# Performance work log

Hardware: AMD Instinct MI355X
Metric: run time of the kernel (lower is better)

The kernel has to match this reference:

```python
import jax, jax.numpy as jnp
import numpy as np

H = 12        # heads
D = 768       # d_model
DK = D // H   # per-head dim
B, S = 1, 4096


def setup_inputs() -> dict:
    key = jax.random.key(0)
    ks = jax.random.split(key, 8)
    scale = 1.0 / np.sqrt(D)
    return {
        "q": jax.random.normal(ks[0], (B, S, D), jnp.float32),
        "k": jax.random.normal(ks[1], (B, S, D), jnp.float32),
        "v": jax.random.normal(ks[2], (B, S, D), jnp.float32),
        "Wq": jax.random.normal(ks[3], (D, D), jnp.float32) * scale,
        "bq": jnp.zeros((D,), jnp.float32),
        "Wk": jax.random.normal(ks[4], (D, D), jnp.float32) * scale,
        "bk": jnp.zeros((D,), jnp.float32),
        "Wv": jax.random.normal(ks[5], (D, D), jnp.float32) * scale,
        "bv": jnp.zeros((D,), jnp.float32),
        "Wo": jax.random.normal(ks[6], (D, D), jnp.float32) * scale,
        "bo": jnp.zeros((D,), jnp.float32),
    }


def reference(q, k, v, Wq, bq, Wk, bk, Wv, bv, Wo, bo):
    bs, sq, _ = q.shape
    sk = k.shape[1]
    # projections, then split heads: (b, h, s, dk)
    qh = (q @ Wq + bq).reshape(bs, sq, H, DK).transpose(0, 2, 1, 3)
    kh = (k @ Wk + bk).reshape(bs, sk, H, DK).transpose(0, 2, 1, 3)
    vh = (v @ Wv + bv).reshape(bs, sk, H, DK).transpose(0, 2, 1, 3)
    # scaled dot-product attention (mask=None, dropout inactive)
    scores = jnp.einsum("bhqd,bhkd->bhqk", qh, kh) / jnp.sqrt(jnp.float32(DK))
    attn = jax.nn.softmax(scores, axis=-1)
    ctx = jnp.einsum("bhqk,bhkd->bhqd", attn, vh)
    concat = ctx.transpose(0, 2, 1, 3).reshape(bs, sq, D)
    return concat @ Wo + bo
```

## Files before the change

kernel.cpp:

```cpp
#include <hip/hip_runtime.h>
#include <hip/hip_bf16.h>


constexpr int S_LEN = 4096;
constexpr int D_MODEL = 768;
constexpr int N_HEADS = 12;
constexpr int D_HEAD = 64;
constexpr int SEG = 2;
constexpr int SEG_LEN = S_LEN / SEG;
constexpr int NITER = SEG_LEN / 64;

#define QSCALE 0.180336880111120f

typedef _Float16 f16;
typedef __attribute__((ext_vector_type(8))) _Float16 f16x8;
typedef __attribute__((ext_vector_type(4))) _Float16 f16x4;
typedef __attribute__((ext_vector_type(4))) float f32x4;

__global__ __launch_bounds__(256) void prep_kernel(
    const float* __restrict__ q, const float* __restrict__ k,
    const float* __restrict__ v, f16* __restrict__ qh,
    f16* __restrict__ kh, f16* __restrict__ vh,
    const float* __restrict__ W0, const float* __restrict__ W1,
    const float* __restrict__ W2, const float* __restrict__ W3,
    f16* __restrict__ WtBase)
{
    __shared__ float T[64][65];
    int bid = blockIdx.x;
    const int t = threadIdx.x;
    if (bid < 4608) {
        int g = bid / 1536, r = bid % 1536;
        const float* x = (g == 0) ? q : (g == 1) ? k : v;
        f16* y = (g == 0) ? qh : (g == 1) ? kh : vh;
        int i = (r * 256 + t) * 8;
        float4 a = *(const float4*)&x[i];
        float4 b = *(const float4*)&x[i + 4];
        f16x8 h = { (f16)a.x, (f16)a.y, (f16)a.z, (f16)a.w,
                    (f16)b.x, (f16)b.y, (f16)b.z, (f16)b.w };
        *(f16x8*)&y[i] = h;
        return;
    }
    bid -= 4608;
    int g = bid / 144, r = bid % 144;
    const float* W = (g == 0) ? W0 : (g == 1) ? W1 : (g == 2) ? W2 : W3;
    f16* Wt = WtBase + (size_t)g * D_MODEL * D_MODEL;
    const int r0 = (r / 12) * 64;
    const int c0 = (r % 12) * 64;
    #pragma unroll
    for (int i = 0; i < 16; ++i) {
        int e = t + 256 * i; int rr = e >> 6, cc = e & 63;
        T[rr][cc] = W[(size_t)(r0 + rr) * D_MODEL + c0 + cc];
    }
    __syncthreads();
    #pragma unroll
    for (int i = 0; i < 16; ++i) {
        int e = t + 256 * i; int rr = e >> 6, cc = e & 63;
        Wt[(size_t)(c0 + rr) * D_MODEL + r0 + cc] = (f16)T[cc][rr];
    }
}

#define GSTR 72

__device__ __forceinline__ void gemm128_core(
    const f16* __restrict__ A, const f16* __restrict__ B,
    f16* As, f16* Bs, int K, int row0, int col0, int t, f32x4 acc[4][4])
{
    const int w = t >> 6, l = t & 63, quad = l >> 4, l15 = l & 15;
    const int wm = (w & 1) * 64, wn = (w >> 1) * 64;

    f16x8 pa[4], pb[4];
    #pragma unroll
    for (int i = 0; i < 4; ++i) {
        int idx = i * 256 + t;
        int r = idx >> 3, c = (idx & 7) * 8;
        pa[i] = *(const f16x8*)&A[(size_t)(row0 + r) * K + c];
        pb[i] = *(const f16x8*)&B[(size_t)(col0 + r) * K + c];
    }

    for (int k0 = 0; k0 < K; k0 += 64) {
        __syncthreads();
        #pragma unroll
        for (int i = 0; i < 4; ++i) {
            int idx = i * 256 + t;
            int r = idx >> 3, c = (idx & 7) * 8;
            *(f16x8*)&As[r * GSTR + c] = pa[i];
            *(f16x8*)&Bs[r * GSTR + c] = pb[i];
        }
        __syncthreads();

        int kn = k0 + 64;
        if (kn < K) {
            #pragma unroll
            for (int i = 0; i < 4; ++i) {
                int idx = i * 256 + t;
                int r = idx >> 3, c = (idx & 7) * 8;
                pa[i] = *(const f16x8*)&A[(size_t)(row0 + r) * K + kn + c];
                pb[i] = *(const f16x8*)&B[(size_t)(col0 + r) * K + kn + c];
            }
        }

        #pragma unroll
        for (int kc = 0; kc < 2; ++kc) {
            f16x8 af[4], bf[4];
            #pragma unroll
            for (int mt = 0; mt < 4; ++mt)
                af[mt] = *(f16x8*)&As[(wm + mt * 16 + l15) * GSTR + kc * 32 + quad * 8];
            #pragma unroll
            for (int nt = 0; nt < 4; ++nt)
                bf[nt] = *(f16x8*)&Bs[(wn + nt * 16 + l15) * GSTR + kc * 32 + quad * 8];
            #pragma unroll
            for (int mt = 0; mt < 4; ++mt)
                #pragma unroll
                for (int nt = 0; nt < 4; ++nt)
                    acc[mt][nt] = __builtin_amdgcn_mfma_f32_16x16x32_f16(
                        af[mt], bf[nt], acc[mt][nt], 0, 0, 0);
        }
    }
}

__global__ __launch_bounds__(256) void qkv_gemm_kernel(
    const f16* __restrict__ qh, const f16* __restrict__ kh,
    const f16* __restrict__ vh, const f16* __restrict__ WtBase,
    const float* __restrict__ bq, const float* __restrict__ bk,
    const float* __restrict__ bv,
    f16* __restrict__ Qp, f16* __restrict__ Kp, f16* __restrict__ Vpt)
{
    __shared__ f16 As[128 * GSTR];
    __shared__ f16 Bs[128 * GSTR];
    const size_t DD = (size_t)D_MODEL * D_MODEL;
    int bid = blockIdx.x;
    int g = bid / 192, r = bid % 192;

    const f16 *A, *B; const float* bias; f16* Y;
    int N; bool biasRow; float scale;
    int row0, col0;
    if (g == 0) {
        A = qh; B = WtBase; bias = bq; Y = Qp;
        N = D_MODEL; biasRow = false; scale = QSCALE;
        row0 = (r / 6) * 128; col0 = (r % 6) * 128;
    } else if (g == 1) {
        A = kh; B = WtBase + DD; bias = bk; Y = Kp;
        N = D_MODEL; biasRow = false; scale = 1.0f;
        row0 = (r / 6) * 128; col0 = (r % 6) * 128;
    } else {
        A = WtBase + 2 * DD; B = vh; bias = bv; Y = Vpt;
        N = S_LEN; biasRow = true; scale = 1.0f;
        row0 = (r / 32) * 128; col0 = (r % 32) * 128;
    }

    f32x4 acc[4][4];
    #pragma unroll
    for (int i = 0; i < 4; ++i)
        #pragma unroll
        for (int j = 0; j < 4; ++j) acc[i][j] = (f32x4){0.f, 0.f, 0.f, 0.f};

    const int t = threadIdx.x;
    gemm128_core(A, B, As, Bs, D_MODEL, row0, col0, t, acc);

    const int w = t >> 6, l = t & 63, quad = l >> 4, l15 = l & 15;
    const int wm = (w & 1) * 64, wn = (w >> 1) * 64;
    #pragma unroll
    for (int mt = 0; mt < 4; ++mt) {
        #pragma unroll
        for (int nt = 0; nt < 4; ++nt) {
            int col = col0 + wn + nt * 16 + l15;
            #pragma unroll
            for (int reg = 0; reg < 4; ++reg) {
                int row = row0 + wm + mt * 16 + quad * 4 + reg;
                float b = biasRow ? bias[row] : bias[col];
                Y[(size_t)row * N + col] = (f16)((acc[mt][nt][reg] + b) * scale);
            }
        }
    }
}

#define LSTR 72

__global__ __launch_bounds__(256, 4) void flash_attn_part_kernel(
    const f16* __restrict__ Q, const f16* __restrict__ K,
    const f16* __restrict__ Vg, f16* __restrict__ Opart,
    float* __restrict__ lsum)
{
    __shared__ f16 Ks[2][64 * LSTR];
    __shared__ f16 Vt[2][64 * LSTR];

    const int t    = threadIdx.x;
    const int w    = t >> 6;
    const int l    = t & 63;
    const int quad = l >> 4;
    const int l15  = l & 15;
    const int h    = blockIdx.y;
    const int q0   = blockIdx.x * 128;
    const int seg  = blockIdx.z;
    const int c0   = h * D_HEAD;
    const size_t SD = (size_t)S_LEN * D_MODEL;

    const int sr = t >> 3;
    const int sc = (t & 7) * 8;
    const int srk = ((sr & 4) << 2) | ((sr & 24) >> 1) | (sr & 3);

    f16x8 qa[2][2];
    #pragma unroll
    for (int qt = 0; qt < 2; ++qt) {
        const f16* qrow = Q + (size_t)(q0 + w * 32 + qt * 16 + l15) * D_MODEL + c0;
        qa[qt][0] = *(const f16x8*)&qrow[quad * 8];
        qa[qt][1] = *(const f16x8*)&qrow[32 + quad * 8];
    }

    f32x4 ctx[2][4];
    float lAcc[2] = {0.f, 0.f};
    #pragma unroll
    for (int qt = 0; qt < 2; ++qt)
        #pragma unroll
        for (int i = 0; i < 4; ++i) ctx[qt][i] = (f32x4){0.f, 0.f, 0.f, 0.f};

    const int kt0 = seg * SEG_LEN;

    f16x8 kreg[2], vreg[2];
    #pragma unroll
    for (int i = 0; i < 2; ++i) {
        int r = i * 32 + sr;
        kreg[i] = *(const f16x8*)&K[(size_t)(kt0 + r) * D_MODEL + c0 + sc];
        vreg[i] = *(const f16x8*)&Vg[(size_t)(c0 + r) * S_LEN + kt0 + sc];
    }
    #pragma unroll
    for (int i = 0; i < 2; ++i) {
        int r = i * 32 + sr;
        *(f16x8*)&Ks[0][(i * 32 + srk) * LSTR + sc] = kreg[i];
        *(f16x8*)&Vt[0][r * LSTR + sc] = vreg[i];
    }
    __syncthreads();
    #pragma unroll
    for (int i = 0; i < 2; ++i) {
        int r = i * 32 + sr;
        kreg[i] = *(const f16x8*)&K[(size_t)(kt0 + 64 + r) * D_MODEL + c0 + sc];
        vreg[i] = *(const f16x8*)&Vg[(size_t)(c0 + r) * S_LEN + kt0 + 64 + sc];
    }

    for (int it = 0; it < NITER; ++it) {
        const int buf = it & 1;
        const f16* ks = Ks[buf];
        const f16* vt = Vt[buf];

        f16x8 pf[2][2];
        #pragma unroll
        for (int s = 0; s < 4; ++s) {
            const int kslot = s >> 1, half = s & 1;
            const f16* kr = &ks[(kslot * 32 + half * 16 + l15) * LSTR];
            f16x8 kb0 = *(const f16x8*)&kr[quad * 8];
            f16x8 kb1 = *(const f16x8*)&kr[32 + quad * 8];
            #pragma unroll
            for (int qt = 0; qt < 2; ++qt) {
                f32x4 z = (f32x4){0.f, 0.f, 0.f, 0.f};
                z = __builtin_amdgcn_mfma_f32_16x16x32_f16(kb0, qa[qt][0], z, 0, 0, 0);
                z = __builtin_amdgcn_mfma_f32_16x16x32_f16(kb1, qa[qt][1], z, 0, 0, 0);
                float p0 = __builtin_amdgcn_exp2f(z[0]);
                float p1 = __builtin_amdgcn_exp2f(z[1]);
                float p2 = __builtin_amdgcn_exp2f(z[2]);
                float p3 = __builtin_amdgcn_exp2f(z[3]);
                lAcc[qt] += (p0 + p1) + (p2 + p3);
                pf[qt][kslot][half * 4 + 0] = (f16)p0;
                pf[qt][kslot][half * 4 + 1] = (f16)p1;
                pf[qt][kslot][half * 4 + 2] = (f16)p2;
                pf[qt][kslot][half * 4 + 3] = (f16)p3;
            }
        }

        #pragma unroll
        for (int mt = 0; mt < 4; ++mt) {
            #pragma unroll
            for (int ks2 = 0; ks2 < 2; ++ks2) {
                f16x8 va = *(const f16x8*)&vt[(mt * 16 + l15) * LSTR + ks2 * 32 + quad * 8];
                #pragma unroll
                for (int qt = 0; qt < 2; ++qt)
                    ctx[qt][mt] = __builtin_amdgcn_mfma_f32_16x16x32_f16(
                        va, pf[qt][ks2], ctx[qt][mt], 0, 0, 0);
            }
        }

        if (it + 1 < NITER) {
            #pragma unroll
            for (int i = 0; i < 2; ++i) {
                int r = i * 32 + sr;
                *(f16x8*)&Ks[1 - buf][(i * 32 + srk) * LSTR + sc] = kreg[i];
                *(f16x8*)&Vt[1 - buf][r * LSTR + sc] = vreg[i];
            }
        }
        __syncthreads();

        if (it + 2 < NITER) {
            int ktn = kt0 + (it + 2) * 64;
            #pragma unroll
            for (int i = 0; i < 2; ++i) {
                int r = i * 32 + sr;
                kreg[i] = *(const f16x8*)&K[(size_t)(ktn + r) * D_MODEL + c0 + sc];
                vreg[i] = *(const f16x8*)&Vg[(size_t)(c0 + r) * S_LEN + ktn + sc];
            }
        }
    }

    #pragma unroll
    for (int qt = 0; qt < 2; ++qt) {
        int qrow = q0 + w * 32 + qt * 16 + l15;
        #pragma unroll
        for (int mt = 0; mt < 4; ++mt) {
            f16x4 ov = { (f16)ctx[qt][mt][0], (f16)ctx[qt][mt][1],
                         (f16)ctx[qt][mt][2], (f16)ctx[qt][mt][3] };
            *(f16x4*)&Opart[(size_t)seg * SD + (size_t)qrow * D_MODEL
                            + c0 + mt * 16 + quad * 4] = ov;
        }
        float s = lAcc[qt];
        s += __shfl_xor(s, 16);
        s += __shfl_xor(s, 32);
        if (quad == 0)
            lsum[((size_t)seg * N_HEADS + h) * S_LEN + qrow] = s;
    }
}

__global__ __launch_bounds__(256) void combine_kernel(
    const f16* __restrict__ Opart, const float* __restrict__ lsum,
    f16* __restrict__ Ctx)
{
    const size_t SD = (size_t)S_LEN * D_MODEL;
    int tid = blockIdx.x * 256 + threadIdx.x;
    int idx = tid * 8;
    int row = idx / D_MODEL;
    int c   = idx % D_MODEL;
    int h   = c >> 6;
    float l0 = lsum[(size_t)h * S_LEN + row];
    float l1 = lsum[((size_t)N_HEADS + h) * S_LEN + row];
    float inv = 1.0f / (l0 + l1);
    f16x8 o0 = *(const f16x8*)&Opart[(size_t)row * D_MODEL + c];
    f16x8 o1 = *(const f16x8*)&Opart[SD + (size_t)row * D_MODEL + c];
    f16x8 r;
    #pragma unroll
    for (int j = 0; j < 8; ++j)
        r[j] = (f16)(((float)o0[j] + (float)o1[j]) * inv);
    *(f16x8*)&Ctx[(size_t)row * D_MODEL + c] = r;
}

__global__ __launch_bounds__(256) void oproj_kernel(
    const f16* __restrict__ Ctx, const f16* __restrict__ Wto,
    const float* __restrict__ bo, float* __restrict__ out)
{
    __shared__ f16 As[128 * GSTR];
    __shared__ f16 Bs[128 * GSTR];
    int bid = blockIdx.x;
    int row0 = (bid / 6) * 128, col0 = (bid % 6) * 128;

    f32x4 acc[4][4];
    #pragma unroll
    for (int i = 0; i < 4; ++i)
        #pragma unroll
        for (int j = 0; j < 4; ++j) acc[i][j] = (f32x4){0.f, 0.f, 0.f, 0.f};

    const int t = threadIdx.x;
    gemm128_core(Ctx, Wto, As, Bs, D_MODEL, row0, col0, t, acc);

    const int w = t >> 6, l = t & 63, quad = l >> 4, l15 = l & 15;
    const int wm = (w & 1) * 64, wn = (w >> 1) * 64;
    #pragma unroll
    for (int mt = 0; mt < 4; ++mt) {
        #pragma unroll
        for (int nt = 0; nt < 4; ++nt) {
            int col = col0 + wn + nt * 16 + l15;
            float b = bo[col];
            #pragma unroll
            for (int reg = 0; reg < 4; ++reg) {
                int row = row0 + wm + mt * 16 + quad * 4 + reg;
                out[(size_t)row * D_MODEL + col] = acc[mt][nt][reg] + b;
            }
        }
    }
}

extern "C" void kernel_launch(void* const* d_in, const int* in_sizes, int n_in,
                              void* d_out, int out_size, void* d_ws, size_t ws_size,
                              hipStream_t stream)
{
    const float* q  = (const float*)d_in[0];
    const float* k  = (const float*)d_in[1];
    const float* v  = (const float*)d_in[2];
    const float* Wq = (const float*)d_in[3];
    const float* bq = (const float*)d_in[4];
    const float* Wk = (const float*)d_in[5];
    const float* bk = (const float*)d_in[6];
    const float* Wv = (const float*)d_in[7];
    const float* bv = (const float*)d_in[8];
    const float* Wo = (const float*)d_in[9];
    const float* bo = (const float*)d_in[10];
    float* out = (float*)d_out;

    const size_t SD = (size_t)S_LEN * D_MODEL;
    const size_t DD = (size_t)D_MODEL * D_MODEL;
    f16* base   = (f16*)d_ws;
    f16* WtBase = base;
    f16* Wto    = WtBase + 3 * DD;
    f16* Qp     = base + 4 * DD;
    f16* Kp     = Qp + SD;
    f16* Vpt    = Kp + SD;
    f16* qh     = Vpt + SD;
    f16* kh     = qh + SD;
    f16* vh     = kh + SD;
    f16* Opart  = qh;
    f16* Ctx    = qh + 2 * SD;
    float* lsum = (float*)(base + 4 * DD + 6 * SD);

    prep_kernel<<<3 * 1536 + 4 * 144, 256, 0, stream>>>(
        q, k, v, qh, kh, vh, Wq, Wk, Wv, Wo, WtBase);

    qkv_gemm_kernel<<<3 * 192, 256, 0, stream>>>(
        qh, kh, vh, WtBase, bq, bk, bv, Qp, Kp, Vpt);

    dim3 gAttn(S_LEN / 128, N_HEADS, SEG);
    flash_attn_part_kernel<<<gAttn, 256, 0, stream>>>(Qp, Kp, Vpt, Opart, lsum);

    combine_kernel<<<1536, 256, 0, stream>>>(Opart, lsum, Ctx);

    oproj_kernel<<<192, 256, 0, stream>>>(Ctx, Wto, bo, out);
}
```

Before: 210.0 us.

## Split attention into four key segments with 32-key tiles and higher occupancy

Attention now uses 32-key tiles instead of 64, which halves the shared-memory K/V buffers, and the occupancy hint rises from 4 to 6 blocks per CU. The number of key segments becomes a runtime value, set to 4 when the workspace is large enough, so the grid has more blocks to fill the GPU. The combine kernel sums a variable number of partials and writes the result in place into segment 0's buffer. The cost is a larger partial buffer and combine traffic, plus twice as many barriers per key, each covering less MFMA work.

```diff
diff --git a/kernel.cpp b/kernel.cpp
--- a/kernel.cpp
+++ b/kernel.cpp
@@ -6,9 +6,6 @@
 constexpr int D_MODEL = 768;
 constexpr int N_HEADS = 12;
 constexpr int D_HEAD = 64;
-constexpr int SEG = 2;
-constexpr int SEG_LEN = S_LEN / SEG;
-constexpr int NITER = SEG_LEN / 64;
 
 #define QSCALE 0.180336880111120f
 
@@ -174,15 +171,16 @@
     }
 }
 
-#define LSTR 72
-
-__global__ __launch_bounds__(256, 4) void flash_attn_part_kernel(
+#define LSTRK 72
+#define VSTR  36
+
+__global__ __launch_bounds__(256, 6) void flash_attn_part_kernel(
     const f16* __restrict__ Q, const f16* __restrict__ K,
     const f16* __restrict__ Vg, f16* __restrict__ Opart,
-    float* __restrict__ lsum)
-{
-    __shared__ f16 Ks[2][64 * LSTR];
-    __shared__ f16 Vt[2][64 * LSTR];
+    float* __restrict__ lsum, int seg_len)
+{
+    __shared__ f16 Ks[2][32 * LSTRK];
+    __shared__ f16 Vt[2][64 * VSTR];
 
     const int t    = threadIdx.x;
     const int w    = t >> 6;
@@ -194,10 +192,13 @@
     const int seg  = blockIdx.z;
     const int c0   = h * D_HEAD;
     const size_t SD = (size_t)S_LEN * D_MODEL;
-
-    const int sr = t >> 3;
-    const int sc = (t & 7) * 8;
+    const int NIT  = seg_len >> 5;
+
+    const int sr  = t >> 3;
+    const int sc  = (t & 7) * 8;
     const int srk = ((sr & 4) << 2) | ((sr & 24) >> 1) | (sr & 3);
+    const int svr = t >> 2;
+    const int svc = (t & 3) * 8;
 
     f16x8 qa[2][2];
     #pragma unroll
@@ -214,39 +215,26 @@
         #pragma unroll
         for (int i = 0; i < 4; ++i) ctx[qt][i] = (f32x4){0.f, 0.f, 0.f, 0.f};
 
-    const int kt0 = seg * SEG_LEN;
-
-    f16x8 kreg[2], vreg[2];
-    #pragma unroll
-    for (int i = 0; i < 2; ++i) {
-        int r = i * 32 + sr;
-        kreg[i] = *(const f16x8*)&K[(size_t)(kt0 + r) * D_MODEL + c0 + sc];
-        vreg[i] = *(const f16x8*)&Vg[(size_t)(c0 + r) * S_LEN + kt0 + sc];
-    }
-    #pragma unroll
-    for (int i = 0; i < 2; ++i) {
-        int r = i * 32 + sr;
-        *(f16x8*)&Ks[0][(i * 32 + srk) * LSTR + sc] = kreg[i];
-        *(f16x8*)&Vt[0][r * LSTR + sc] = vreg[i];
-    }
+    const int kt0 = seg * seg_len;
+
+    f16x8 kreg, vreg;
+    kreg = *(const f16x8*)&K[(size_t)(kt0 + sr) * D_MODEL + c0 + sc];
+    vreg = *(const f16x8*)&Vg[(size_t)(c0 + svr) * S_LEN + kt0 + svc];
+    *(f16x8*)&Ks[0][srk * LSTRK + sc] = kreg;
+    *(f16x8*)&Vt[0][svr * VSTR + svc] = vreg;
     __syncthreads();
-    #pragma unroll
-    for (int i = 0; i < 2; ++i) {
-        int r = i * 32 + sr;
-        kreg[i] = *(const f16x8*)&K[(size_t)(kt0 + 64 + r) * D_MODEL + c0 + sc];
-        vreg[i] = *(const f16x8*)&Vg[(size_t)(c0 + r) * S_LEN + kt0 + 64 + sc];
-    }
-
-    for (int it = 0; it < NITER; ++it) {
+    kreg = *(const f16x8*)&K[(size_t)(kt0 + 32 + sr) * D_MODEL + c0 + sc];
+    vreg = *(const f16x8*)&Vg[(size_t)(c0 + svr) * S_LEN + kt0 + 32 + svc];
+
+    for (int it = 0; it < NIT; ++it) {
         const int buf = it & 1;
         const f16* ks = Ks[buf];
         const f16* vt = Vt[buf];
 
-        f16x8 pf[2][2];
-        #pragma unroll
-        for (int s = 0; s < 4; ++s) {
-            const int kslot = s >> 1, half = s & 1;
-            const f16* kr = &ks[(kslot * 32 + half * 16 + l15) * LSTR];
+        f16x8 pf[2];
+        #pragma unroll
+        for (int half = 0; half < 2; ++half) {
+            const f16* kr = &ks[(half * 16 + l15) * LSTRK];
             f16x8 kb0 = *(const f16x8*)&kr[quad * 8];
             f16x8 kb1 = *(const f16x8*)&kr[32 + quad * 8];
             #pragma unroll
@@ -259,43 +247,32 @@
                 float p2 = __builtin_amdgcn_exp2f(z[2]);
                 float p3 = __builtin_amdgcn_exp2f(z[3]);
                 lAcc[qt] += (p0 + p1) + (p2 + p3);
-                pf[qt][kslot][half * 4 + 0] = (f16)p0;
-                pf[qt][kslot][half * 4 + 1] = (f16)p1;
-                pf[qt][kslot][half * 4 + 2] = (f16)p2;
-                pf[qt][kslot][half * 4 + 3] = (f16)p3;
+                pf[qt][half * 4 + 0] = (f16)p0;
+                pf[qt][half * 4 + 1] = (f16)p1;
+                pf[qt][half * 4 + 2] = (f16)p2;
+                pf[qt][half * 4 + 3] = (f16)p3;
             }
         }
 
         #pragma unroll
         for (int mt = 0; mt < 4; ++mt) {
-            #pragma unroll
-            for (int ks2 = 0; ks2 < 2; ++ks2) {
-                f16x8 va = *(const f16x8*)&vt[(mt * 16 + l15) * LSTR + ks2 * 32 + quad * 8];
-                #pragma unroll
-                for (int qt = 0; qt < 2; ++qt)
-                    ctx[qt][mt] = __builtin_amdgcn_mfma_f32_16x16x32_f16(
-                        va, pf[qt][ks2], ctx[qt][mt], 0, 0, 0);
-            }
-        }
-
-        if (it + 1 < NITER) {
-            #pragma unroll
-            for (int i = 0; i < 2; ++i) {
-                int r = i * 32 + sr;
-                *(f16x8*)&Ks[1 - buf][(i * 32 + srk) * LSTR + sc] = kreg[i];
-                *(f16x8*)&Vt[1 - buf][r * LSTR + sc] = vreg[i];
-            }
+            f16x8 va = *(const f16x8*)&vt[(mt * 16 + l15) * VSTR + quad * 8];
+            #pragma unroll
+            for (int qt = 0; qt < 2; ++qt)
+                ctx[qt][mt] = __builtin_amdgcn_mfma_f32_16x16x32_f16(
+                    va, pf[qt], ctx[qt][mt], 0, 0, 0);
+        }
+
+        if (it + 1 < NIT) {
+            *(f16x8*)&Ks[1 - buf][srk * LSTRK + sc] = kreg;
+            *(f16x8*)&Vt[1 - buf][svr * VSTR + svc] = vreg;
         }
         __syncthreads();
 
-        if (it + 2 < NITER) {
-            int ktn = kt0 + (it + 2) * 64;
-            #pragma unroll
-            for (int i = 0; i < 2; ++i) {
-                int r = i * 32 + sr;
-                kreg[i] = *(const f16x8*)&K[(size_t)(ktn + r) * D_MODEL + c0 + sc];
-                vreg[i] = *(const f16x8*)&Vg[(size_t)(c0 + r) * S_LEN + ktn + sc];
-            }
+        if (it + 2 < NIT) {
+            int ktn = kt0 + (it + 2) * 32;
+            kreg = *(const f16x8*)&K[(size_t)(ktn + sr) * D_MODEL + c0 + sc];
+            vreg = *(const f16x8*)&Vg[(size_t)(c0 + svr) * S_LEN + ktn + svc];
         }
     }
 
@@ -318,25 +295,29 @@
 }
 
 __global__ __launch_bounds__(256) void combine_kernel(
-    const f16* __restrict__ Opart, const float* __restrict__ lsum,
-    f16* __restrict__ Ctx)
+    f16* Opart, const float* __restrict__ lsum, int nseg)
 {
     const size_t SD = (size_t)S_LEN * D_MODEL;
     int tid = blockIdx.x * 256 + threadIdx.x;
     int idx = tid * 8;
     int row = idx / D_MODEL;
     int c   = idx % D_MODEL;
-    int h   = c >> 6;
-    float l0 = lsum[(size_t)h * S_LEN + row];
-    float l1 = lsum[((size_t)N_HEADS + h) * S_LEN + row];
-    float inv = 1.0f / (l0 + l1);
-    f16x8 o0 = *(const f16x8*)&Opart[(size_t)row * D_MODEL + c];
-    f16x8 o1 = *(const f16x8*)&Opart[SD + (size_t)row * D_MODEL + c];
+    int hh  = c >> 6;
+    float lt = 0.f;
+    for (int s = 0; s < nseg; ++s)
+        lt += lsum[((size_t)s * N_HEADS + hh) * S_LEN + row];
+    float inv = 1.0f / lt;
+    float o[8] = {0.f, 0.f, 0.f, 0.f, 0.f, 0.f, 0.f, 0.f};
+    for (int s = 0; s < nseg; ++s) {
+        f16x8 os = *(const f16x8*)&Opart[(size_t)s * SD + (size_t)row * D_MODEL + c];
+        #pragma unroll
+        for (int j = 0; j < 8; ++j) o[j] += (float)os[j];
+    }
     f16x8 r;
     #pragma unroll
     for (int j = 0; j < 8; ++j)
-        r[j] = (f16)(((float)o0[j] + (float)o1[j]) * inv);
-    *(f16x8*)&Ctx[(size_t)row * D_MODEL + c] = r;
+        r[j] = (f16)(o[j] * inv);
+    *(f16x8*)&Opart[(size_t)row * D_MODEL + c] = r;
 }
 
 __global__ __launch_bounds__(256) void oproj_kernel(
@@ -403,8 +384,12 @@
     f16* kh     = qh + SD;
     f16* vh     = kh + SD;
     f16* Opart  = qh;
-    f16* Ctx    = qh + 2 * SD;
-    float* lsum = (float*)(base + 4 * DD + 6 * SD);
+
+    const size_t need4 = (4 * DD + 7 * SD) * sizeof(f16)
+                       + 4 * (size_t)N_HEADS * S_LEN * sizeof(float);
+    const int nseg = (ws_size >= need4) ? 4 : 2;
+    const int seg_len = S_LEN / nseg;
+    float* lsum = (float*)(base + 4 * DD + (3 + (size_t)nseg) * SD);
 
     prep_kernel<<<3 * 1536 + 4 * 144, 256, 0, stream>>>(
         q, k, v, qh, kh, vh, Wq, Wk, Wv, Wo, WtBase);
@@ -412,10 +397,11 @@
     qkv_gemm_kernel<<<3 * 192, 256, 0, stream>>>(
         qh, kh, vh, WtBase, bq, bk, bv, Qp, Kp, Vpt);
 
-    dim3 gAttn(S_LEN / 128, N_HEADS, SEG);
-    flash_attn_part_kernel<<<gAttn, 256, 0, stream>>>(Qp, Kp, Vpt, Opart, lsum);
-
-    combine_kernel<<<1536, 256, 0, stream>>>(Opart, lsum, Ctx);
-
-    oproj_kernel<<<192, 256, 0, stream>>>(Ctx, Wto, bo, out);
-}
+    dim3 gAttn(S_LEN / 128, N_HEADS, nseg);
+    flash_attn_part_kernel<<<gAttn, 256, 0, stream>>>(
+        Qp, Kp, Vpt, Opart, lsum, seg_len);
+
+    combine_kernel<<<1536, 256, 0, stream>>>(Opart, lsum, nseg);
+
+    oproj_kernel<<<192, 256, 0, stream>>>(Opart, Wto, bo, out);
+}
```

Measured after the change: 335.2 us. +59.6%, slower.

## Fuse fp32→fp16 input conversion into QKV GEMM and split-combine into O-proj loads

Applied to the files above, without the earlier changes.

The separate pass that converted q/k/v from fp32 to fp16 is removed. The QKV GEMM now loads fp32 tiles directly and converts them in registers. The combine kernel is also removed: the output-projection GEMM reads both partial attention outputs plus the lsum values and normalizes them while loading its A operand. This cuts two kernel launches and several full S×D intermediate round trips through global memory. In exchange the GEMM loads fetch twice the bytes for fp32 operands, and the O-proj repeats the combine work for each of its 6 column tiles, with extra lsum loads and divides.

```diff
diff --git a/kernel.cpp b/kernel.cpp
--- a/kernel.cpp
+++ b/kernel.cpp
@@ -18,9 +18,6 @@
 typedef __attribute__((ext_vector_type(4))) float f32x4;
 
 __global__ __launch_bounds__(256) void prep_kernel(
-    const float* __restrict__ q, const float* __restrict__ k,
-    const float* __restrict__ v, f16* __restrict__ qh,
-    f16* __restrict__ kh, f16* __restrict__ vh,
     const float* __restrict__ W0, const float* __restrict__ W1,
     const float* __restrict__ W2, const float* __restrict__ W3,
     f16* __restrict__ WtBase)
@@ -28,19 +25,6 @@
     __shared__ float T[64][65];
     int bid = blockIdx.x;
     const int t = threadIdx.x;
-    if (bid < 4608) {
-        int g = bid / 1536, r = bid % 1536;
-        const float* x = (g == 0) ? q : (g == 1) ? k : v;
-        f16* y = (g == 0) ? qh : (g == 1) ? kh : vh;
-        int i = (r * 256 + t) * 8;
-        float4 a = *(const float4*)&x[i];
-        float4 b = *(const float4*)&x[i + 4];
-        f16x8 h = { (f16)a.x, (f16)a.y, (f16)a.z, (f16)a.w,
-                    (f16)b.x, (f16)b.y, (f16)b.z, (f16)b.w };
-        *(f16x8*)&y[i] = h;
-        return;
-    }
-    bid -= 4608;
     int g = bid / 144, r = bid % 144;
     const float* W = (g == 0) ? W0 : (g == 1) ? W1 : (g == 2) ? W2 : W3;
     f16* Wt = WtBase + (size_t)g * D_MODEL * D_MODEL;
@@ -61,21 +45,59 @@
 
 #define GSTR 72
 
-__device__ __forceinline__ void gemm128_core(
-    const f16* __restrict__ A, const f16* __restrict__ B,
+template<int AM, int BM>
+__device__ __forceinline__ void gemm128_core_t(
+    const f16* A16, const float* Af, const f16* A16b, const float* ls,
+    const f16* B16, const float* Bf,
     f16* As, f16* Bs, int K, int row0, int col0, int t, f32x4 acc[4][4])
 {
     const int w = t >> 6, l = t & 63, quad = l >> 4, l15 = l & 15;
     const int wm = (w & 1) * 64, wn = (w >> 1) * 64;
 
     f16x8 pa[4], pb[4];
-    #pragma unroll
-    for (int i = 0; i < 4; ++i) {
+
+    auto loadA = [&](int i, int kk) {
         int idx = i * 256 + t;
         int r = idx >> 3, c = (idx & 7) * 8;
-        pa[i] = *(const f16x8*)&A[(size_t)(row0 + r) * K + c];
-        pb[i] = *(const f16x8*)&B[(size_t)(col0 + r) * K + c];
-    }
+        if constexpr (AM == 0) {
+            pa[i] = *(const f16x8*)&A16[(size_t)(row0 + r) * K + kk + c];
+        } else if constexpr (AM == 1) {
+            const float* p = &Af[(size_t)(row0 + r) * K + kk + c];
+            float4 a = *(const float4*)p;
+            float4 b = *(const float4*)(p + 4);
+            pa[i] = (f16x8){ (f16)a.x, (f16)a.y, (f16)a.z, (f16)a.w,
+                             (f16)b.x, (f16)b.y, (f16)b.z, (f16)b.w };
+        } else {
+            int R = row0 + r;
+            f16x8 a0 = *(const f16x8*)&A16[(size_t)R * K + kk + c];
+            f16x8 a1 = *(const f16x8*)&A16b[(size_t)R * K + kk + c];
+            int hh = (kk + c) >> 6;
+            float lt = ls[(size_t)hh * S_LEN + R]
+                     + ls[(size_t)(N_HEADS + hh) * S_LEN + R];
+            float inv = 1.0f / lt;
+            f16x8 o;
+            #pragma unroll
+            for (int j = 0; j < 8; ++j)
+                o[j] = (f16)(((float)a0[j] + (float)a1[j]) * inv);
+            pa[i] = o;
+        }
+    };
+    auto loadB = [&](int i, int kk) {
+        int idx = i * 256 + t;
+        int r = idx >> 3, c = (idx & 7) * 8;
+        if constexpr (BM == 0) {
+            pb[i] = *(const f16x8*)&B16[(size_t)(col0 + r) * K + kk + c];
+        } else {
+            const float* p = &Bf[(size_t)(col0 + r) * K + kk + c];
+            float4 a = *(const float4*)p;
+            float4 b = *(const float4*)(p + 4);
+            pb[i] = (f16x8){ (f16)a.x, (f16)a.y, (f16)a.z, (f16)a.w,
+                             (f16)b.x, (f16)b.y, (f16)b.z, (f16)b.w };
+        }
+    };
+
+    #pragma unroll
+    for (int i = 0; i < 4; ++i) { loadA(i, 0); loadB(i, 0); }
 
     for (int k0 = 0; k0 < K; k0 += 64) {
         __syncthreads();
@@ -91,12 +113,7 @@
         int kn = k0 + 64;
         if (kn < K) {
             #pragma unroll
-            for (int i = 0; i < 4; ++i) {
-                int idx = i * 256 + t;
-                int r = idx >> 3, c = (idx & 7) * 8;
-                pa[i] = *(const f16x8*)&A[(size_t)(row0 + r) * K + kn + c];
-                pb[i] = *(const f16x8*)&B[(size_t)(col0 + r) * K + kn + c];
-            }
+            for (int i = 0; i < 4; ++i) { loadA(i, kn); loadB(i, kn); }
         }
 
         #pragma unroll
@@ -119,8 +136,8 @@
 }
 
 __global__ __launch_bounds__(256) void qkv_gemm_kernel(
-    const f16* __restrict__ qh, const f16* __restrict__ kh,
-    const f16* __restrict__ vh, const f16* __restrict__ WtBase,
+    const float* __restrict__ q, const float* __restrict__ k,
+    const float* __restrict__ v, const f16* __restrict__ WtBase,
     const float* __restrict__ bq, const float* __restrict__ bk,
     const float* __restrict__ bv,
     f16* __restrict__ Qp, f16* __restrict__ Kp, f16* __restrict__ Vpt)
@@ -130,32 +147,33 @@
     const size_t DD = (size_t)D_MODEL * D_MODEL;
     int bid = blockIdx.x;
     int g = bid / 192, r = bid % 192;
-
-    const f16 *A, *B; const float* bias; f16* Y;
+    const int t = threadIdx.x;
+
+    f32x4 acc[4][4];
+    #pragma unroll
+    for (int i = 0; i < 4; ++i)
+        #pragma unroll
+        for (int j = 0; j < 4; ++j) acc[i][j] = (f32x4){0.f, 0.f, 0.f, 0.f};
+
+    const float* bias; f16* Y;
     int N; bool biasRow; float scale;
     int row0, col0;
     if (g == 0) {
-        A = qh; B = WtBase; bias = bq; Y = Qp;
-        N = D_MODEL; biasRow = false; scale = QSCALE;
         row0 = (r / 6) * 128; col0 = (r % 6) * 128;
+        gemm128_core_t<1, 0>(nullptr, q, nullptr, nullptr, WtBase, nullptr,
+                             As, Bs, D_MODEL, row0, col0, t, acc);
+        bias = bq; Y = Qp; N = D_MODEL; biasRow = false; scale = QSCALE;
     } else if (g == 1) {
-        A = kh; B = WtBase + DD; bias = bk; Y = Kp;
-        N = D_MODEL; biasRow = false; scale = 1.0f;
         row0 = (r / 6) * 128; col0 = (r % 6) * 128;
+        gemm128_core_t<1, 0>(nullptr, k, nullptr, nullptr, WtBase + DD, nullptr,
+                             As, Bs, D_MODEL, row0, col0, t, acc);
+        bias = bk; Y = Kp; N = D_MODEL; biasRow = false; scale = 1.0f;
     } else {
-        A = WtBase + 2 * DD; B = vh; bias = bv; Y = Vpt;
-        N = S_LEN; biasRow = true; scale = 1.0f;
         row0 = (r / 32) * 128; col0 = (r % 32) * 128;
-    }
-
-    f32x4 acc[4][4];
-    #pragma unroll
-    for (int i = 0; i < 4; ++i)
-        #pragma unroll
-        for (int j = 0; j < 4; ++j) acc[i][j] = (f32x4){0.f, 0.f, 0.f, 0.f};
-
-    const int t = threadIdx.x;
-    gemm128_core(A, B, As, Bs, D_MODEL, row0, col0, t, acc);
+        gemm128_core_t<0, 1>(WtBase + 2 * DD, nullptr, nullptr, nullptr, nullptr, v,
+                             As, Bs, D_MODEL, row0, col0, t, acc);
+        bias = bv; Y = Vpt; N = S_LEN; biasRow = true; scale = 1.0f;
+    }
 
     const int w = t >> 6, l = t & 63, quad = l >> 4, l15 = l & 15;
     const int wm = (w & 1) * 64, wn = (w >> 1) * 64;
@@ -317,34 +335,14 @@
     }
 }
 
-__global__ __launch_bounds__(256) void combine_kernel(
+__global__ __launch_bounds__(256) void oproj_kernel(
     const f16* __restrict__ Opart, const float* __restrict__ lsum,
-    f16* __restrict__ Ctx)
-{
-    const size_t SD = (size_t)S_LEN * D_MODEL;
-    int tid = blockIdx.x * 256 + threadIdx.x;
-    int idx = tid * 8;
-    int row = idx / D_MODEL;
-    int c   = idx % D_MODEL;
-    int h   = c >> 6;
-    float l0 = lsum[(size_t)h * S_LEN + row];
-    float l1 = lsum[((size_t)N_HEADS + h) * S_LEN + row];
-    float inv = 1.0f / (l0 + l1);
-    f16x8 o0 = *(const f16x8*)&Opart[(size_t)row * D_MODEL + c];
-    f16x8 o1 = *(const f16x8*)&Opart[SD + (size_t)row * D_MODEL + c];
-    f16x8 r;
-    #pragma unroll
-    for (int j = 0; j < 8; ++j)
-        r[j] = (f16)(((float)o0[j] + (float)o1[j]) * inv);
-    *(f16x8*)&Ctx[(size_t)row * D_MODEL + c] = r;
-}
-
-__global__ __launch_bounds__(256) void oproj_kernel(
-    const f16* __restrict__ Ctx, const f16* __restrict__ Wto,
-    const float* __restrict__ bo, float* __restrict__ out)
+    const f16* __restrict__ Wto, const float* __restrict__ bo,
+    float* __restrict__ out)
 {
     __shared__ f16 As[128 * GSTR];
     __shared__ f16 Bs[128 * GSTR];
+    const size_t SD = (size_t)S_LEN * D_MODEL;
     int bid = blockIdx.x;
     int row0 = (bid / 6) * 128, col0 = (bid % 6) * 128;
 
@@ -355,7 +353,8 @@
         for (int j = 0; j < 4; ++j) acc[i][j] = (f32x4){0.f, 0.f, 0.f, 0.f};
 
     const int t = threadIdx.x;
-    gemm128_core(Ctx, Wto, As, Bs, D_MODEL, row0, col0, t, acc);
+    gemm128_core_t<2, 0>(Opart, nullptr, Opart + SD, lsum, Wto, nullptr,
+                         As, Bs, D_MODEL, row0, col0, t, acc);
 
     const int w = t >> 6, l = t & 63, quad = l >> 4, l15 = l & 15;
     const int wm = (w & 1) * 64, wn = (w >> 1) * 64;
@@ -399,23 +398,16 @@
     f16* Qp     = base + 4 * DD;
     f16* Kp     = Qp + SD;
     f16* Vpt    = Kp + SD;
-    f16* qh     = Vpt + SD;
-    f16* kh     = qh + SD;
-    f16* vh     = kh + SD;
-    f16* Opart  = qh;
-    f16* Ctx    = qh + 2 * SD;
-    float* lsum = (float*)(base + 4 * DD + 6 * SD);
-
-    prep_kernel<<<3 * 1536 + 4 * 144, 256, 0, stream>>>(
-        q, k, v, qh, kh, vh, Wq, Wk, Wv, Wo, WtBase);
+    f16* Opart  = Vpt + SD;
+    float* lsum = (float*)(base + 4 * DD + 5 * SD);
+
+    prep_kernel<<<4 * 144, 256, 0, stream>>>(Wq, Wk, Wv, Wo, WtBase);
 
     qkv_gemm_kernel<<<3 * 192, 256, 0, stream>>>(
-        qh, kh, vh, WtBase, bq, bk, bv, Qp, Kp, Vpt);
+        q, k, v, WtBase, bq, bk, bv, Qp, Kp, Vpt);
 
     dim3 gAttn(S_LEN / 128, N_HEADS, SEG);
     flash_attn_part_kernel<<<gAttn, 256, 0, stream>>>(Qp, Kp, Vpt, Opart, lsum);
 
-    combine_kernel<<<1536, 256, 0, stream>>>(Opart, lsum, Ctx);
-
-    oproj_kernel<<<192, 256, 0, stream>>>(Ctx, Wto, bo, out);
-}
+    oproj_kernel<<<192, 256, 0, stream>>>(Opart, lsum, Wto, bo, out);
+}
```

Result: slower. 231.1 us (+10.0%).
